# Kernel tuning notes

Hardware: AMD Instinct MI355X
Metric: run time of the kernel (lower is better)

Reference implementation:

```python
import jax, jax.numpy as jnp
import numpy as np
from jax import lax

SIGMA_S = 60.0
SIGMA_R = 0.4
ITER_NUM = 2
SQRT2 = 1.4142135623730951
SQRT3 = 1.7320508075688772


def _linrec_op(l, r):
    # combine two affine maps x -> a*x + b applied in sequence (l first, then r)
    al, bl = l
    ar, br = r
    return (al * ar, ar * bl + br)


def _recursive_filter(img, D, sigma):
    """Domain-transform recursive filter along the last axis (width).
    Forward pass:  x_i = V_i * x_{i-1} + (1 - V_i) * img_i,  x_0 = img_0
    Backward pass: y_i = V_{i+1} * y_{i+1} + (1 - V_{i+1}) * x_i, y_{w-1} = x_{w-1}
    img: [B,C,H,W], D: [B,1,H,W]
    """
    a = jnp.exp(jnp.float32(-SQRT2 / sigma))
    V = jnp.broadcast_to(a ** D, img.shape)  # [B,C,H,W]

    # left-to-right linear recurrence via parallel associative scan
    af = V.at[..., 0].set(0.0)  # x_0 = img_0
    bf = (1.0 - af) * img
    _, x = lax.associative_scan(_linrec_op, (af, bf), axis=-1)

    # right-to-left pass: coefficient at position i is V[i+1]; flip, scan, flip back
    ab = jnp.concatenate([V[..., 1:], jnp.zeros_like(V[..., :1])], axis=-1)
    ab = ab[..., ::-1]
    bb = (1.0 - ab) * x[..., ::-1]
    _, y = lax.associative_scan(_linrec_op, (ab, bb), axis=-1)
    return y[..., ::-1]


def setup_inputs() -> dict:
    key = jax.random.key(0)
    k1, k2 = jax.random.split(key)
    img = jax.random.normal(k1, (4, 32, 512, 512), dtype=jnp.float32)
    edge = jax.random.uniform(k2, (4, 1, 512, 512), dtype=jnp.float32)
    return {"img": img, "edge": edge}


def reference(img, edge):
    dHdx = 1.0 + (SIGMA_S / SIGMA_R) * edge            # [B,1,H,W]
    dVdy = jnp.swapaxes(dHdx, 2, 3)                    # [B,1,W,H]
    denom = float(np.sqrt(4.0 ** ITER_NUM - 1.0))
    for i in range(ITER_NUM):
        sigma_i = SIGMA_S * SQRT3 * (2.0 ** (ITER_NUM - (i + 1))) / denom
        img = _recursive_filter(img, dHdx, sigma_i)    # filter along W
        img = jnp.swapaxes(img, 2, 3)
        img = _recursive_filter(img, dVdy, sigma_i)    # filter along H
        img = jnp.swapaxes(img, 2, 3)
    return img
```

## Files before the change

kernel.cpp:

```cpp
#include <hip/hip_runtime.h>

#define C0F (-0.026352313834736496f)
#define C1F (-0.052704627669472993f)

#define NB 4
#define NC 32
#define NH 512
#define NW 512

typedef _Float16 h16;
typedef __attribute__((ext_vector_type(8))) _Float16 f16x8;

__device__ __forceinline__ void load8(const float* p, float* x) {
    float4 a = *reinterpret_cast<const float4*>(p);
    float4 b = *reinterpret_cast<const float4*>(p + 4);
    x[0]=a.x; x[1]=a.y; x[2]=a.z; x[3]=a.w;
    x[4]=b.x; x[5]=b.y; x[6]=b.z; x[7]=b.w;
}
__device__ __forceinline__ void load8(const h16* p, float* x) {
    f16x8 h = *reinterpret_cast<const f16x8*>(p);
    #pragma unroll
    for (int i = 0; i < 8; ++i) x[i] = (float)h[i];
}
__device__ __forceinline__ void store8(float* p, const float* x) {
    *reinterpret_cast<float4*>(p)     = make_float4(x[0],x[1],x[2],x[3]);
    *reinterpret_cast<float4*>(p + 4) = make_float4(x[4],x[5],x[6],x[7]);
}
__device__ __forceinline__ void store8(h16* p, const float* x) {
    f16x8 h;
    #pragma unroll
    for (int i = 0; i < 8; ++i) h[i] = (h16)x[i];
    *reinterpret_cast<f16x8*>(p) = h;
}

__device__ __forceinline__ void row_scan(float (&x)[8], const float (&v)[8], int lane) {
    float A = 1.f, Bv = 0.f;
    #pragma unroll
    for (int i = 0; i < 8; ++i) {
        float a = v[i];
        if (lane == 0 && i == 0) a = 0.f;
        Bv = a * Bv + (1.f - a) * x[i];
        A *= a;
    }
    #pragma unroll
    for (int d = 1; d < 64; d <<= 1) {
        float Ap = __shfl_up(A, d);
        float Bp = __shfl_up(Bv, d);
        if (lane >= d) { Bv = A * Bp + Bv; A *= Ap; }
    }
    float carry = __shfl_up(Bv, 1);
    if (lane == 0) carry = 0.f;
    float xp = carry;
    #pragma unroll
    for (int i = 0; i < 8; ++i) {
        float a = v[i];
        if (lane == 0 && i == 0) a = 0.f;
        xp = a * xp + (1.f - a) * x[i];
        x[i] = xp;
    }
    float vn = __shfl_down(v[0], 1);
    float A2 = 1.f, B2 = 0.f;
    #pragma unroll
    for (int i = 7; i >= 0; --i) {
        float a = (i < 7) ? v[i + 1] : ((lane == 63) ? 0.f : vn);
        B2 = a * B2 + (1.f - a) * x[i];
        A2 *= a;
    }
    #pragma unroll
    for (int d = 1; d < 64; d <<= 1) {
        float Ap = __shfl_down(A2, d);
        float Bp = __shfl_down(B2, d);
        if (lane < 64 - d) { B2 = A2 * Bp + B2; A2 *= Ap; }
    }
    float cb = __shfl_down(B2, 1);
    if (lane == 63) cb = 0.f;
    float yn = cb;
    #pragma unroll
    for (int i = 7; i >= 0; --i) {
        float a = (i < 7) ? v[i + 1] : ((lane == 63) ? 0.f : vn);
        yn = a * yn + (1.f - a) * x[i];
        x[i] = yn;
    }
}

template <typename ST, typename DT>
__global__ void __launch_bounds__(512, 8)
rs_pass(const ST* __restrict__ src, DT* __restrict__ dst,
        const float* __restrict__ vt) {
    __shared__ h16 tile[32 * 512];
    const int lane = threadIdx.x & 63;
    const int wv   = threadIdx.x >> 6;
    const int bc   = blockIdx.x >> 4;
    const int band = blockIdx.x & 15;
    const int b    = bc >> 5;
    const int rho0 = band << 5;
    const ST*    sb = src + ((size_t)bc << 18);
    const float* vb = vt  + ((size_t)b  << 18);

    #pragma unroll
    for (int k = 0; k < 4; ++k) {
        const int r   = (wv << 2) + k;
        const int row = rho0 + r;
        float x[8], v[8];
        load8(sb + ((size_t)row << 9) + (lane << 3), x);
        load8(vb + ((size_t)row << 9) + (lane << 3), v);
        row_scan(x, v, lane);
        f16x8 hx;
        #pragma unroll
        for (int i = 0; i < 8; ++i) hx[i] = (h16)x[i];
        const int cc = (((lane << 3) + ((r >> 3) << 4)) & 511);
        *reinterpret_cast<f16x8*>(&tile[r * 512 + cc]) = hx;
    }
    __syncthreads();
    const int g = lane >> 2;
    const int j = lane & 3;
    #pragma unroll
    for (int m = 0; m < 4; ++m) {
        const int c = (wv << 6) + (m << 4) + g;
        float y[8];
        #pragma unroll
        for (int k = 0; k < 8; ++k) {
            const int rr = (j << 3) + k;
            y[k] = (float)tile[rr * 512 + ((c + (j << 4)) & 511)];
        }
        store8(dst + ((size_t)bc << 18) + ((size_t)c << 9) + rho0 + (j << 3), y);
    }
}

__global__ __launch_bounds__(256) void vtab_t_kernel(const float* __restrict__ edge,
                                                     float* __restrict__ v0,
                                                     float* __restrict__ v1,
                                                     float* __restrict__ v0t,
                                                     float* __restrict__ v1t) {
    __shared__ float T0[64][65], T1[64][65];
    const int t  = threadIdx.x;
    const int i  = t & 15;
    const int q  = t >> 4;
    const int b  = blockIdx.x >> 6;
    const int tt = blockIdx.x & 63;
    const int h0 = (tt >> 3) << 6;
    const int w0 = (tt & 7) << 6;
    const size_t ib = (size_t)b << 18;
    #pragma unroll
    for (int rr = 0; rr < 4; ++rr) {
        const int r = q + (rr << 4);
        const size_t off = ib + ((size_t)(h0 + r) << 9) + w0 + (i << 2);
        float4 e = *reinterpret_cast<const float4*>(edge + off);
        float4 a0, a1; float d;
        d = 1.f + 150.f * e.x; a0.x = expf(C0F*d); a1.x = expf(C1F*d);
        d = 1.f + 150.f * e.y; a0.y = expf(C0F*d); a1.y = expf(C1F*d);
        d = 1.f + 150.f * e.z; a0.z = expf(C0F*d); a1.z = expf(C1F*d);
        d = 1.f + 150.f * e.w; a0.w = expf(C0F*d); a1.w = expf(C1F*d);
        *reinterpret_cast<float4*>(v0 + off) = a0;
        *reinterpret_cast<float4*>(v1 + off) = a1;
        const int c = i << 2;
        T0[r][c+0]=a0.x; T0[r][c+1]=a0.y; T0[r][c+2]=a0.z; T0[r][c+3]=a0.w;
        T1[r][c+0]=a1.x; T1[r][c+1]=a1.y; T1[r][c+2]=a1.z; T1[r][c+3]=a1.w;
    }
    __syncthreads();
    #pragma unroll
    for (int rr = 0; rr < 4; ++rr) {
        const int w = q + (rr << 4);
        const int c = i << 2;
        float4 o0, o1;
        o0.x=T0[c+0][w]; o0.y=T0[c+1][w]; o0.z=T0[c+2][w]; o0.w=T0[c+3][w];
        o1.x=T1[c+0][w]; o1.y=T1[c+1][w]; o1.z=T1[c+2][w]; o1.w=T1[c+3][w];
        const size_t off = ib + ((size_t)(w0 + w) << 9) + h0 + c;
        *reinterpret_cast<float4*>(v0t + off) = o0;
        *reinterpret_cast<float4*>(v1t + off) = o1;
    }
}

__global__ __launch_bounds__(256) void vtab_kernel(const float* __restrict__ edge,
                                                   float* __restrict__ v0,
                                                   float* __restrict__ v1) {
    int i = blockIdx.x * 256 + threadIdx.x;
    float4 e = reinterpret_cast<const float4*>(edge)[i];
    float dx = 1.f + 150.f * e.x;
    float dy = 1.f + 150.f * e.y;
    float dz = 1.f + 150.f * e.z;
    float dw = 1.f + 150.f * e.w;
    float4 a0, a1;
    a0.x = expf(C0F * dx); a0.y = expf(C0F * dy); a0.z = expf(C0F * dz); a0.w = expf(C0F * dw);
    a1.x = expf(C1F * dx); a1.y = expf(C1F * dy); a1.z = expf(C1F * dz); a1.w = expf(C1F * dw);
    reinterpret_cast<float4*>(v0)[i] = a0;
    reinterpret_cast<float4*>(v1)[i] = a1;
}

template <typename ST, typename DT>
__global__ __launch_bounds__(256) void hpass_kernel(const ST* __restrict__ src,
                                                    DT* __restrict__ dst,
                                                    const float* __restrict__ vt) {
    const int lane = threadIdx.x & 63;
    const int wv   = threadIdx.x >> 6;
    const int row  = (blockIdx.x << 2) + wv;
    const int h    = row & (NH - 1);
    const int bc   = row >> 9;
    const int b    = bc >> 5;
    const ST* srow = src + ((size_t)row << 9);
    DT*       drow = dst + ((size_t)row << 9);
    const float* vrow = vt + (((size_t)(b << 9) + h) << 9);
    const int g0 = lane << 3;
    float x[8], v[8];
    load8(srow + g0, x);
    load8(vrow + g0, v);
    row_scan(x, v, lane);
    store8(drow + g0, x);
}

#define VROWS 32
template <typename ST, typename DT>
__global__ __launch_bounds__(512) void vpass_kernel(const ST* __restrict__ src,
                                                    DT* __restrict__ dst,
                                                    const float* __restrict__ vt) {
    const int col   = threadIdx.x & 31;
    const int hc    = threadIdx.x >> 5;
    const int strip = blockIdx.x & 15;
    const int bc    = blockIdx.x >> 4;
    const int b     = bc >> 5;
    const int w     = (strip << 5) + col;
    const ST*    sbase = src + ((size_t)bc << 18) + w;
    DT*          dbase = dst + ((size_t)bc << 18) + w;
    const float* vb    = vt  + ((size_t)b  << 18) + w;
    const int h0 = hc << 5;
    float x[VROWS], v[VROWS];
    #pragma unroll
    for (int i = 0; i < VROWS; ++i) x[i] = (float)sbase[(size_t)(h0 + i) << 9];
    #pragma unroll
    for (int i = 0; i < VROWS; ++i) v[i] = vb[(size_t)(h0 + i) << 9];
    __shared__ float sA[16][32], sB[16][32], sC[16][32], sV[16][32];
    float A = 1.f, Bv = 0.f;
    #pragma unroll
    for (int i = 0; i < VROWS; ++i) {
        float a = v[i];
        if (hc == 0 && i == 0) a = 0.f;
        Bv = a * Bv + (1.f - a) * x[i];
        A *= a;
    }
    sA[hc][col] = A; sB[hc][col] = Bv;
    __syncthreads();
    if (hc == 0) {
        float cr = 0.f;
        #pragma unroll
        for (int k = 0; k < 16; ++k) {
            float a_ = sA[k][col], b_ = sB[k][col];
            sC[k][col] = cr;
            cr = a_ * cr + b_;
        }
    }
    __syncthreads();
    float xp = sC[hc][col];
    #pragma unroll
    for (int i = 0; i < VROWS; ++i) {
        float a = v[i];
        if (hc == 0 && i == 0) a = 0.f;
        xp = a * xp + (1.f - a) * x[i];
        x[i] = xp;
    }
    sV[hc][col] = v[0];
    __syncthreads();
    float vnext = (hc < 15) ? sV[hc + 1][col] : 0.f;
    A = 1.f; Bv = 0.f;
    #pragma unroll
    for (int i = VROWS - 1; i >= 0; --i) {
        float a = (i < VROWS - 1) ? v[i + 1] : ((hc == 15) ? 0.f : vnext);
        Bv = a * Bv + (1.f - a) * x[i];
        A *= a;
    }
    sA[hc][col] = A; sB[hc][col] = Bv;
    __syncthreads();
    if (hc == 0) {
        float cr = 0.f;
        #pragma unroll
        for (int k = 15; k >= 0; --k) {
            float a_ = sA[k][col], b_ = sB[k][col];
            sC[k][col] = cr;
            cr = a_ * cr + b_;
        }
    }
    __syncthreads();
    float yn = sC[hc][col];
    #pragma unroll
    for (int i = VROWS - 1; i >= 0; --i) {
        float a = (i < VROWS - 1) ? v[i + 1] : ((hc == 15) ? 0.f : vnext);
        yn = a * yn + (1.f - a) * x[i];
        x[i] = yn;
    }
    #pragma unroll
    for (int i = 0; i < VROWS; ++i) dbase[(size_t)(h0 + i) << 9] = (DT)x[i];
}

extern "C" void kernel_launch(void* const* d_in, const int* in_sizes, int n_in,
                              void* d_out, int out_size, void* d_ws, size_t ws_size,
                              hipStream_t stream) {
    const float* img  = (const float*)d_in[0];
    const float* edge = (const float*)d_in[1];
    float* out = (float*)d_out;

    const size_t NBHW = (size_t)NB * NH * NW;
    const size_t NTOT = (size_t)NB * NC * NH * NW;
    float* v0  = (float*)d_ws;
    float* v1  = v0  + NBHW;
    float* v0t = v1  + NBHW;
    float* v1t = v0t + NBHW;
    h16*   tA  = (h16*)(v1t + NBHW);
    h16*   tB  = tA + NTOT;
    const size_t needMain = NBHW * 16 + NTOT * 4;
    const size_t needT2   = NBHW * 8  + NTOT * 2;

    if (ws_size >= needMain) {
        vtab_t_kernel<<<NB * 64, 256, 0, stream>>>(edge, v0, v1, v0t, v1t);
        const int G = NB * NC * 16;
        rs_pass<float, h16><<<G, 512, 0, stream>>>(img, tA, v0);
        rs_pass<h16,  h16><<<G, 512, 0, stream>>>(tA, tB, v0t);
        rs_pass<h16,  h16><<<G, 512, 0, stream>>>(tB, tA, v1);
        rs_pass<h16, float><<<G, 512, 0, stream>>>(tA, out, v1t);
    } else if (ws_size >= needT2) {
        h16* tmp = (h16*)(v0t);
        vtab_kernel<<<(int)(NBHW / (256 * 4)), 256, 0, stream>>>(edge, v0, v1);
        const int HG = NB * NC * NH / 4;
        const int VG = NB * NC * (NW / 32);
        hpass_kernel<float, h16><<<HG, 256, 0, stream>>>(img, tmp, v0);
        vpass_kernel<h16, h16><<<VG, 512, 0, stream>>>(tmp, tmp, v0);
        hpass_kernel<h16, h16><<<HG, 256, 0, stream>>>(tmp, tmp, v1);
        vpass_kernel<h16, float><<<VG, 512, 0, stream>>>(tmp, out, v1);
    } else {
        vtab_kernel<<<(int)(NBHW / (256 * 4)), 256, 0, stream>>>(edge, v0, v1);
        const int HG = NB * NC * NH / 4;
        const int VG = NB * NC * (NW / 32);
        hpass_kernel<float, float><<<HG, 256, 0, stream>>>(img, out, v0);
        vpass_kernel<float, float><<<VG, 512, 0, stream>>>(out, out, v0);
        hpass_kernel<float, float><<<HG, 256, 0, stream>>>(out, out, v1);
        vpass_kernel<float, float><<<VG, 512, 0, stream>>>(out, out, v1);
    }
}
```

Before: 172.1 us.

## Process rows with half-wave scans and double the transposed tile per block

The row-scan-and-transpose kernel now splits each 64-lane wave into two 32-lane halves, and each half scans a full 512-wide row with 16 elements per lane. Each block now handles a 64-row band instead of 32, so the grid halves. Writes go out as 32-element contiguous runs per output row, and LDS reads use paired fp16 loads. The aim is fewer shuffle steps per row, wider coalesced stores and fewer blocks, at the cost of doubled LDS per block (64 KB), lower occupancy and more registers.

```diff
diff --git a/kernel.cpp b/kernel.cpp
--- a/kernel.cpp
+++ b/kernel.cpp
@@ -10,6 +10,7 @@
 
 typedef _Float16 h16;
 typedef __attribute__((ext_vector_type(8))) _Float16 f16x8;
+typedef __attribute__((ext_vector_type(2))) _Float16 f16x2;
 
 __device__ __forceinline__ void load8(const float* p, float* x) {
     float4 a = *reinterpret_cast<const float4*>(p);
@@ -32,98 +33,112 @@
     for (int i = 0; i < 8; ++i) h[i] = (h16)x[i];
     *reinterpret_cast<f16x8*>(p) = h;
 }
-
-__device__ __forceinline__ void row_scan(float (&x)[8], const float (&v)[8], int lane) {
-    float A = 1.f, Bv = 0.f;
-    #pragma unroll
-    for (int i = 0; i < 8; ++i) {
-        float a = v[i];
-        if (lane == 0 && i == 0) a = 0.f;
-        Bv = a * Bv + (1.f - a) * x[i];
+template <typename ST>
+__device__ __forceinline__ void load16(const ST* p, float (&x)[16]) {
+    load8(p, x); load8(p + 8, x + 8);
+}
+template <typename DT>
+__device__ __forceinline__ void store16(DT* p, const float (&y)[16]) {
+    store8(p, y); store8(p + 8, y + 8);
+}
+
+__device__ __forceinline__ void row_scan32(float (&x)[16], const float (&v)[16], int u) {
+    float A = 1.f, B = 0.f;
+    #pragma unroll
+    for (int i = 0; i < 16; ++i) {
+        float a = v[i];
+        if (u == 0 && i == 0) a = 0.f;
+        B = a * B + (1.f - a) * x[i];
         A *= a;
     }
     #pragma unroll
-    for (int d = 1; d < 64; d <<= 1) {
-        float Ap = __shfl_up(A, d);
-        float Bp = __shfl_up(Bv, d);
-        if (lane >= d) { Bv = A * Bp + Bv; A *= Ap; }
-    }
-    float carry = __shfl_up(Bv, 1);
-    if (lane == 0) carry = 0.f;
+    for (int d = 1; d < 32; d <<= 1) {
+        float Ap = __shfl_up(A, d, 32);
+        float Bp = __shfl_up(B, d, 32);
+        if (u >= d) { B = A * Bp + B; A *= Ap; }
+    }
+    float carry = __shfl_up(B, 1, 32);
+    if (u == 0) carry = 0.f;
     float xp = carry;
     #pragma unroll
-    for (int i = 0; i < 8; ++i) {
-        float a = v[i];
-        if (lane == 0 && i == 0) a = 0.f;
+    for (int i = 0; i < 16; ++i) {
+        float a = v[i];
+        if (u == 0 && i == 0) a = 0.f;
         xp = a * xp + (1.f - a) * x[i];
         x[i] = xp;
     }
-    float vn = __shfl_down(v[0], 1);
+    float vn = __shfl_down(v[0], 1, 32);
     float A2 = 1.f, B2 = 0.f;
     #pragma unroll
-    for (int i = 7; i >= 0; --i) {
-        float a = (i < 7) ? v[i + 1] : ((lane == 63) ? 0.f : vn);
+    for (int i = 15; i >= 0; --i) {
+        float a = (i < 15) ? v[i + 1] : ((u == 31) ? 0.f : vn);
         B2 = a * B2 + (1.f - a) * x[i];
         A2 *= a;
     }
     #pragma unroll
-    for (int d = 1; d < 64; d <<= 1) {
-        float Ap = __shfl_down(A2, d);
-        float Bp = __shfl_down(B2, d);
-        if (lane < 64 - d) { B2 = A2 * Bp + B2; A2 *= Ap; }
-    }
-    float cb = __shfl_down(B2, 1);
-    if (lane == 63) cb = 0.f;
+    for (int d = 1; d < 32; d <<= 1) {
+        float Ap = __shfl_down(A2, d, 32);
+        float Bp = __shfl_down(B2, d, 32);
+        if (u < 32 - d) { B2 = A2 * Bp + B2; A2 *= Ap; }
+    }
+    float cb = __shfl_down(B2, 1, 32);
+    if (u == 31) cb = 0.f;
     float yn = cb;
     #pragma unroll
-    for (int i = 7; i >= 0; --i) {
-        float a = (i < 7) ? v[i + 1] : ((lane == 63) ? 0.f : vn);
+    for (int i = 15; i >= 0; --i) {
+        float a = (i < 15) ? v[i + 1] : ((u == 31) ? 0.f : vn);
         yn = a * yn + (1.f - a) * x[i];
         x[i] = yn;
     }
 }
 
 template <typename ST, typename DT>
-__global__ void __launch_bounds__(512, 8)
+__global__ void __launch_bounds__(512, 4)
 rs_pass(const ST* __restrict__ src, DT* __restrict__ dst,
         const float* __restrict__ vt) {
-    __shared__ h16 tile[32 * 512];
+    __shared__ h16 tile[64 * 512];
     const int lane = threadIdx.x & 63;
     const int wv   = threadIdx.x >> 6;
-    const int bc   = blockIdx.x >> 4;
-    const int band = blockIdx.x & 15;
+    const int bc   = blockIdx.x >> 3;
+    const int band = blockIdx.x & 7;
     const int b    = bc >> 5;
-    const int rho0 = band << 5;
+    const int rho0 = band << 6;
     const ST*    sb = src + ((size_t)bc << 18);
     const float* vb = vt  + ((size_t)b  << 18);
 
+    const int u    = lane & 31;
+    const int half = lane >> 5;
     #pragma unroll
     for (int k = 0; k < 4; ++k) {
-        const int r   = (wv << 2) + k;
+        const int r   = (wv << 3) + (k << 1) + half;
         const int row = rho0 + r;
-        float x[8], v[8];
-        load8(sb + ((size_t)row << 9) + (lane << 3), x);
-        load8(vb + ((size_t)row << 9) + (lane << 3), v);
-        row_scan(x, v, lane);
-        f16x8 hx;
+        float x[16], v[16];
+        load16(sb + ((size_t)row << 9) + (u << 4), x);
+        load16(vb + ((size_t)row << 9) + (u << 4), v);
+        row_scan32(x, v, u);
+        const int csw = ((u + (r >> 4)) & 31) << 4;
+        h16* tp = &tile[r * 512 + csw];
+        store8(tp, x);
+        store8(tp + 8, x + 8);
+    }
+    __syncthreads();
+    const int t = lane >> 2;
+    const int j = lane & 3;
+    #pragma unroll
+    for (int m = 0; m < 2; ++m) {
+        const int c0 = (wv << 6) + (m << 5) + (t << 1);
+        const int cb = (c0 + (j << 4)) & 511;
+        float y0[16], y1[16];
         #pragma unroll
-        for (int i = 0; i < 8; ++i) hx[i] = (h16)x[i];
-        const int cc = (((lane << 3) + ((r >> 3) << 4)) & 511);
-        *reinterpret_cast<f16x8*>(&tile[r * 512 + cc]) = hx;
-    }
-    __syncthreads();
-    const int g = lane >> 2;
-    const int j = lane & 3;
-    #pragma unroll
-    for (int m = 0; m < 4; ++m) {
-        const int c = (wv << 6) + (m << 4) + g;
-        float y[8];
-        #pragma unroll
-        for (int k = 0; k < 8; ++k) {
-            const int rr = (j << 3) + k;
-            y[k] = (float)tile[rr * 512 + ((c + (j << 4)) & 511)];
+        for (int k = 0; k < 16; ++k) {
+            f16x2 p = *reinterpret_cast<const f16x2*>(
+                &tile[(((j << 4) + k) << 9) + cb]);
+            y0[k] = (float)p[0];
+            y1[k] = (float)p[1];
         }
-        store8(dst + ((size_t)bc << 18) + ((size_t)c << 9) + rho0 + (j << 3), y);
+        DT* dp = dst + ((size_t)bc << 18) + ((size_t)c0 << 9) + rho0 + (j << 4);
+        store16(dp, y0);
+        store16(dp + NH, y1);
     }
 }
 
@@ -185,6 +200,56 @@
     a1.x = expf(C1F * dx); a1.y = expf(C1F * dy); a1.z = expf(C1F * dz); a1.w = expf(C1F * dw);
     reinterpret_cast<float4*>(v0)[i] = a0;
     reinterpret_cast<float4*>(v1)[i] = a1;
+}
+
+__device__ __forceinline__ void row_scan(float (&x)[8], const float (&v)[8], int lane) {
+    float A = 1.f, Bv = 0.f;
+    #pragma unroll
+    for (int i = 0; i < 8; ++i) {
+        float a = v[i];
+        if (lane == 0 && i == 0) a = 0.f;
+        Bv = a * Bv + (1.f - a) * x[i];
+        A *= a;
+    }
+    #pragma unroll
+    for (int d = 1; d < 64; d <<= 1) {
+        float Ap = __shfl_up(A, d);
+        float Bp = __shfl_up(Bv, d);
+        if (lane >= d) { Bv = A * Bp + Bv; A *= Ap; }
+    }
+    float carry = __shfl_up(Bv, 1);
+    if (lane == 0) carry = 0.f;
+    float xp = carry;
+    #pragma unroll
+    for (int i = 0; i < 8; ++i) {
+        float a = v[i];
+        if (lane == 0 && i == 0) a = 0.f;
+        xp = a * xp + (1.f - a) * x[i];
+        x[i] = xp;
+    }
+    float vn = __shfl_down(v[0], 1);
+    float A2 = 1.f, B2 = 0.f;
+    #pragma unroll
+    for (int i = 7; i >= 0; --i) {
+        float a = (i < 7) ? v[i + 1] : ((lane == 63) ? 0.f : vn);
+        B2 = a * B2 + (1.f - a) * x[i];
+        A2 *= a;
+    }
+    #pragma unroll
+    for (int d = 1; d < 64; d <<= 1) {
+        float Ap = __shfl_down(A2, d);
+        float Bp = __shfl_down(B2, d);
+        if (lane < 64 - d) { B2 = A2 * Bp + B2; A2 *= Ap; }
+    }
+    float cb = __shfl_down(B2, 1);
+    if (lane == 63) cb = 0.f;
+    float yn = cb;
+    #pragma unroll
+    for (int i = 7; i >= 0; --i) {
+        float a = (i < 7) ? v[i + 1] : ((lane == 63) ? 0.f : vn);
+        yn = a * yn + (1.f - a) * x[i];
+        x[i] = yn;
+    }
 }
 
 template <typename ST, typename DT>
@@ -310,7 +375,7 @@
 
     if (ws_size >= needMain) {
         vtab_t_kernel<<<NB * 64, 256, 0, stream>>>(edge, v0, v1, v0t, v1t);
-        const int G = NB * NC * 16;
+        const int G = NB * NC * 8;
         rs_pass<float, h16><<<G, 512, 0, stream>>>(img, tA, v0);
         rs_pass<h16,  h16><<<G, 512, 0, stream>>>(tA, tB, v0t);
         rs_pass<h16,  h16><<<G, 512, 0, stream>>>(tB, tA, v1);
```

Measured after the change: 192.3 us. 11.8% more time.
